# Performance work log

Hardware: AMD Instinct MI355X
Metric: run time of the kernel (lower is better)

The kernel has to match this reference:

```python
import jax, jax.numpy as jnp
import numpy as np

H = 128  # hidden size
I = 256  # input size

def setup_inputs() -> dict:
    key = jax.random.key(0)
    ks = jax.random.split(key, 12)
    s_ih = 1.0 / np.sqrt(H)
    inp = {
        "x": jax.random.normal(ks[0], (256, 512, I), dtype=jnp.float32),
        # PyTorch LSTM params, gate order (i, f, g, o)
        "W_ih": jax.random.uniform(ks[1], (4 * H, I), jnp.float32, -s_ih, s_ih),
        "W_hh": jax.random.uniform(ks[2], (4 * H, H), jnp.float32, -s_ih, s_ih),
        "b_ih": jax.random.uniform(ks[3], (4 * H,), jnp.float32, -s_ih, s_ih),
        "b_hh": jax.random.uniform(ks[4], (4 * H,), jnp.float32, -s_ih, s_ih),
        "W1": jax.random.uniform(ks[5], (64, H), jnp.float32, -1/np.sqrt(H), 1/np.sqrt(H)),
        "b1": jax.random.uniform(ks[6], (64,), jnp.float32, -1/np.sqrt(H), 1/np.sqrt(H)),
        "W2": jax.random.uniform(ks[7], (32, 64), jnp.float32, -1/np.sqrt(64), 1/np.sqrt(64)),
        "b2": jax.random.uniform(ks[8], (32,), jnp.float32, -1/np.sqrt(64), 1/np.sqrt(64)),
        "W3": jax.random.uniform(ks[9], (4, 32), jnp.float32, -1/np.sqrt(32), 1/np.sqrt(32)),
        "b3": jax.random.uniform(ks[10], (4,), jnp.float32, -1/np.sqrt(32), 1/np.sqrt(32)),
    }
    return inp

def _lstm_last_hidden(x, W_ih, W_hh, b_ih, b_hh):
    B = x.shape[0]
    # Precompute input contribution for all timesteps: [B, T, 4H]
    gx = jnp.einsum("bti,gi->btg", x, W_ih) + (b_ih + b_hh)
    gx = jnp.swapaxes(gx, 0, 1)  # [T, B, 4H] for scan over time

    def step(carry, g_x):
        h, c = carry
        gates = g_x + h @ W_hh.T  # [B, 4H]
        i, f, g, o = jnp.split(gates, 4, axis=-1)
        i = jax.nn.sigmoid(i)
        f = jax.nn.sigmoid(f)
        g = jnp.tanh(g)
        o = jax.nn.sigmoid(o)
        c = f * c + i * g
        h = o * jnp.tanh(c)
        return (h, c), None

    h0 = jnp.zeros((B, H), x.dtype)
    (h, _), _ = jax.lax.scan(step, (h0, h0), gx)
    return h  # last-timestep hidden state [B, H]

def reference(x, W_ih, W_hh, b_ih, b_hh, W1, b1, W2, b2, W3, b3):
    h = _lstm_last_hidden(x, W_ih, W_hh, b_ih, b_hh)
    h = jax.nn.relu(h @ W1.T + b1)
    h = jax.nn.relu(h @ W2.T + b2)
    return h @ W3.T + b3  # [B, 4]
```

## Files before the change

kernel.cpp:

```cpp
#include <hip/hip_runtime.h>
#include <hip/hip_bf16.h>


#define TC       64
#define NCHUNK   8
#define BATCH    256
#define TSEQ     512
#define ISZ      256
#define HSZ      128
#define RB       4
#define NBLK     (BATCH / RB)
#define NGB      (2 * TC * 4)
#define HROW     144
#define GX_PER_T 131072
#define GXCH     ((size_t)TC * GX_PER_T)
#define STRT     32768
#define PF       4

#define XN       (BATCH * TSEQ * ISZ)
#define WIHN     (4 * HSZ * ISZ)
#define WHHN     (4 * HSZ * HSZ)
#define NCB      ((XN + WIHN + WHHN) / 8192)

typedef __attribute__((ext_vector_type(8))) short short8;
typedef __attribute__((ext_vector_type(4))) float f32x4;

__device__ __forceinline__ void barrier_nodrain() {
    __asm__ __volatile__("s_waitcnt lgkmcnt(0)\n\ts_barrier" ::: "memory");
}

__device__ __forceinline__ float fast_rcp(float x) {
    return __builtin_amdgcn_rcpf(x);
}
__device__ __forceinline__ float sigmoidf_(float x) {
    return fast_rcp(1.0f + __expf(-x));
}
__device__ __forceinline__ float tanhf_(float x) {
    float e = __expf(2.0f * x);
    return 1.0f - 2.0f * fast_rcp(e + 1.0f);
}
__device__ __forceinline__ unsigned short f2bf(float x) {
    union { float f; unsigned u; } v; v.f = x;
    unsigned r = v.u + 0x7fffu + ((v.u >> 16) & 1u);
    return (unsigned short)(r >> 16);
}
__device__ __forceinline__ float bf2f(unsigned short b) {
    union { unsigned u; float f; } v;
    v.u = ((unsigned)b) << 16;
    return v.f;
}
__device__ __forceinline__ unsigned packbf(float lo, float hi) {
    __hip_bfloat162 h2 = __float22bfloat162_rn(make_float2(lo, hi));
    union { __hip_bfloat162 h; unsigned u; } v; v.h = h2;
    return v.u;
}
__device__ __forceinline__ float sel4(f32x4 v, int r) {
    float s01 = (r & 1) ? v[1] : v[0];
    float s23 = (r & 1) ? v[3] : v[2];
    return (r & 2) ? s23 : s01;
}

__global__ __launch_bounds__(512, 2) void fused_kernel(
    const float* __restrict__ x, const float* __restrict__ Wih,
    const float* __restrict__ bih, const float* __restrict__ bhh,
    const float* __restrict__ Whh,
    const unsigned short* __restrict__ gxl, unsigned short* __restrict__ gxg,
    float* __restrict__ hc,
    unsigned short* __restrict__ xb, unsigned short* __restrict__ wihb,
    unsigned short* __restrict__ whhb,
    int t0, int first, int run_lstm, int run_gemm, int use_xbf, int run_conv)
{
    __shared__ __align__(16) char smem[32768];
    const int tid  = threadIdx.x;
    const int w    = tid >> 6;
    const int lane = tid & 63;
    const int n    = lane & 15;
    const int quad = lane >> 4;

    if (blockIdx.x >= NBLK + NGB) {
        if (!run_conv) return;
        const int cb = (int)blockIdx.x - (NBLK + NGB);
        const size_t e0 = ((size_t)cb * 512 + tid) * 16;
        const float* s; unsigned short* d;
        if (e0 < (size_t)XN)              { s = x + e0;                d = xb + e0; }
        else if (e0 < (size_t)(XN + WIHN)){ s = Wih + (e0 - XN);       d = wihb + (e0 - XN); }
        else                              { s = Whh + (e0 - XN - WIHN); d = whhb + (e0 - XN - WIHN); }
        float4 f0 = *(const float4*)(s);
        float4 f1 = *(const float4*)(s + 4);
        float4 f2 = *(const float4*)(s + 8);
        float4 f3 = *(const float4*)(s + 12);
        *(uint4*)(d)     = (uint4){packbf(f0.x, f0.y), packbf(f0.z, f0.w),
                                   packbf(f1.x, f1.y), packbf(f1.z, f1.w)};
        *(uint4*)(d + 8) = (uint4){packbf(f2.x, f2.y), packbf(f2.z, f2.w),
                                   packbf(f3.x, f3.y), packbf(f3.z, f3.w)};
        return;
    }

    if (blockIdx.x >= NBLK) {
        if (!run_gemm) return;
        short* As = (short*)smem;
        short* Bs = (short*)(smem + 16384);

        const int gb = (int)blockIdx.x - NBLK;
        const int nt = gb & 3;
        const int mt = gb >> 2;
        const int tl = mt >> 1;
        const int b0 = (mt & 1) * 128;
        const int n0 = nt * 128;

        const int mq = w & 1;
        const int nq = w >> 1;

        const int srow = tid >> 2;
        const int skh  = (tid & 3) * 8;

        f32x4 acc[4][2];
#pragma unroll
        for (int mi = 0; mi < 4; ++mi)
#pragma unroll
            for (int ni = 0; ni < 2; ++ni)
                acc[mi][ni] = (f32x4){0.f, 0.f, 0.f, 0.f};

        if (use_xbf) {
            const unsigned short* xr = xb + ((size_t)(b0 + srow) * TSEQ + (size_t)(t0 + tl)) * ISZ + skh;
            const unsigned short* wr = wihb + (size_t)(n0 + srow) * ISZ + skh;
            *(short8*)(&As[srow * 32 + skh]) = *(const short8*)(xr);
            *(short8*)(&Bs[srow * 32 + skh]) = *(const short8*)(wr);
            barrier_nodrain();
            for (int ks = 0; ks < 8; ++ks) {
                const int cur = (ks & 1) * 4096;
                const int nxt = 4096 - cur;
                short8 va, vb;
                if (ks < 7) {
                    va = *(const short8*)(xr + (ks + 1) * 32);
                    vb = *(const short8*)(wr + (ks + 1) * 32);
                }
                short8 af[4], bfr[2];
#pragma unroll
                for (int mi = 0; mi < 4; ++mi)
                    af[mi] = *(const short8*)(&As[cur + (mq * 64 + mi * 16 + n) * 32 + quad * 8]);
#pragma unroll
                for (int ni = 0; ni < 2; ++ni)
                    bfr[ni] = *(const short8*)(&Bs[cur + (nq * 32 + ni * 16 + n) * 32 + quad * 8]);
#pragma unroll
                for (int mi = 0; mi < 4; ++mi)
#pragma unroll
                    for (int ni = 0; ni < 2; ++ni)
                        acc[mi][ni] = __builtin_amdgcn_mfma_f32_16x16x32_bf16(
                            af[mi], bfr[ni], acc[mi][ni], 0, 0, 0);
                if (ks < 7) {
                    *(short8*)(&As[nxt + srow * 32 + skh]) = va;
                    *(short8*)(&Bs[nxt + srow * 32 + skh]) = vb;
                }
                barrier_nodrain();
            }
        } else {
            const float* xrow = x + ((size_t)(b0 + srow) * TSEQ + (size_t)(t0 + tl)) * ISZ + skh;
            const float* wrow = Wih + (size_t)(n0 + srow) * ISZ + skh;
            {
                float4 pa0 = *(const float4*)(xrow);
                float4 pa1 = *(const float4*)(xrow + 4);
                float4 pb0 = *(const float4*)(wrow);
                float4 pb1 = *(const float4*)(wrow + 4);
                *(uint4*)(&As[srow * 32 + skh]) =
                    (uint4){packbf(pa0.x, pa0.y), packbf(pa0.z, pa0.w),
                            packbf(pa1.x, pa1.y), packbf(pa1.z, pa1.w)};
                *(uint4*)(&Bs[srow * 32 + skh]) =
                    (uint4){packbf(pb0.x, pb0.y), packbf(pb0.z, pb0.w),
                            packbf(pb1.x, pb1.y), packbf(pb1.z, pb1.w)};
            }
            barrier_nodrain();
            for (int ks = 0; ks < 8; ++ks) {
                const int cur = (ks & 1) * 4096;
                const int nxt = 4096 - cur;
                float4 pa0, pa1, pb0, pb1;
                if (ks < 7) {
                    pa0 = *(const float4*)(xrow + (ks + 1) * 32);
                    pa1 = *(const float4*)(xrow + (ks + 1) * 32 + 4);
                    pb0 = *(const float4*)(wrow + (ks + 1) * 32);
                    pb1 = *(const float4*)(wrow + (ks + 1) * 32 + 4);
                }
                short8 af[4], bfr[2];
#pragma unroll
                for (int mi = 0; mi < 4; ++mi)
                    af[mi] = *(const short8*)(&As[cur + (mq * 64 + mi * 16 + n) * 32 + quad * 8]);
#pragma unroll
                for (int ni = 0; ni < 2; ++ni)
                    bfr[ni] = *(const short8*)(&Bs[cur + (nq * 32 + ni * 16 + n) * 32 + quad * 8]);
#pragma unroll
                for (int mi = 0; mi < 4; ++mi)
#pragma unroll
                    for (int ni = 0; ni < 2; ++ni)
                        acc[mi][ni] = __builtin_amdgcn_mfma_f32_16x16x32_bf16(
                            af[mi], bfr[ni], acc[mi][ni], 0, 0, 0);
                if (ks < 7) {
                    *(uint4*)(&As[nxt + srow * 32 + skh]) =
                        (uint4){packbf(pa0.x, pa0.y), packbf(pa0.z, pa0.w),
                                packbf(pa1.x, pa1.y), packbf(pa1.z, pa1.w)};
                    *(uint4*)(&Bs[nxt + srow * 32 + skh]) =
                        (uint4){packbf(pb0.x, pb0.y), packbf(pb0.z, pb0.w),
                                packbf(pb1.x, pb1.y), packbf(pb1.z, pb1.w)};
                }
                barrier_nodrain();
            }
        }

#pragma unroll
        for (int ni = 0; ni < 2; ++ni) {
            const int j    = nq * 32 + ni * 16 + n;
            const int gate = n0 + j;
            const float bias = bih[gate] + bhh[gate];
            const int wj = nq * 2 + ni;
#pragma unroll
            for (int mi = 0; mi < 4; ++mi) {
                const int bb   = b0 + mq * 64 + mi * 16 + quad * 4;
                const int blk2 = bb >> 2;
                const size_t idx = ((((size_t)nt * TC + tl) * 64 + blk2) * 512) +
                                   (size_t)wj * 64 + (size_t)n * 4;
                const unsigned lo = packbf(acc[mi][ni][0] + bias, acc[mi][ni][1] + bias);
                const unsigned hi = packbf(acc[mi][ni][2] + bias, acc[mi][ni][3] + bias);
                *(uint2*)(&gxg[idx]) = (uint2){lo, hi};
            }
        }
        return;
    }

    if (!run_lstm) return;
    __builtin_amdgcn_s_setprio(1);
    short* h_lds = (short*)smem;

    const int blk  = (int)blockIdx.x;
    const int b0   = blk * RB;
    const int nb   = lane & 3;
    const int jl   = lane >> 2;
    const int j    = 16 * w + jl;
    const int rsel = jl & 3;

    short8 Af[4][4];
#pragma unroll
    for (int g = 0; g < 4; ++g) {
        const unsigned short* rowb = whhb + (size_t)(128 * g + 16 * w + n) * HSZ + 8 * quad;
#pragma unroll
        for (int ks = 0; ks < 4; ++ks)
            Af[g][ks] = *(const short8*)(rowb + 32 * ks);
    }

    float c1 = 0.f, hl1 = 0.f;
    {
        unsigned short h0 = 0;
        if (!first) {
            c1 = hc[(size_t)BATCH * HSZ + (size_t)(b0 + nb) * HSZ + j];
            h0 = f2bf(hc[(size_t)(b0 + nb) * HSZ + j]);
        }
        *(unsigned short*)&h_lds[nb * HROW + j] = h0;
    }

    const unsigned short* gp[4];
#pragma unroll
    for (int g = 0; g < 4; ++g)
        gp[g] = gxl + (((size_t)g * TC) * 64 + blk) * 512 + (size_t)w * 64 + lane;

    unsigned short gq[PF][4];
#pragma unroll
    for (int d = 0; d < PF; ++d)
#pragma unroll
        for (int g = 0; g < 4; ++g)
            gq[d][g] = gp[g][(size_t)d * STRT];

    barrier_nodrain();

    for (int t = 0; t < TC; t += PF) {
#pragma unroll
        for (int u = 0; u < PF; ++u) {
            const int tt = t + u;
            const short* hb_r = h_lds + (u & 1) * (RB * HROW);
            short*       hb_w = h_lds + ((u & 1) ^ 1) * (RB * HROW);

            short8 Bf[4];
#pragma unroll
            for (int ks = 0; ks < 4; ++ks)
                Bf[ks] = *(const short8*)(&hb_r[nb * HROW + 32 * ks + 8 * quad]);

            f32x4 acc[4];
#pragma unroll
            for (int g = 0; g < 4; ++g)
                acc[g] = __builtin_amdgcn_mfma_f32_16x16x32_bf16(
                    Af[g][0], Bf[0], (f32x4){0.f, 0.f, 0.f, 0.f}, 0, 0, 0);
#pragma unroll
            for (int ks = 1; ks < 4; ++ks)
#pragma unroll
                for (int g = 0; g < 4; ++g)
                    acc[g] = __builtin_amdgcn_mfma_f32_16x16x32_bf16(
                        Af[g][ks], Bf[ks], acc[g], 0, 0, 0);

            const float s0 = sel4(acc[0], rsel) + bf2f(gq[u][0]);
            const float s1 = sel4(acc[1], rsel) + bf2f(gq[u][1]);
            const float s2 = sel4(acc[2], rsel) + bf2f(gq[u][2]);
            const float s3 = sel4(acc[3], rsel) + bf2f(gq[u][3]);

            const int tf = (tt + PF < TC) ? (tt + PF) : (TC - 1);
#pragma unroll
            for (int g = 0; g < 4; ++g)
                gq[u][g] = gp[g][(size_t)tf * STRT];

            const float ig = sigmoidf_(s0);
            const float fg = sigmoidf_(s1);
            const float gg = tanhf_(s2);
            const float og = sigmoidf_(s3);
            c1  = fg * c1 + ig * gg;
            hl1 = og * tanhf_(c1);

            *(unsigned short*)&hb_w[nb * HROW + j] = f2bf(hl1);
            barrier_nodrain();
        }
    }

    hc[(size_t)(b0 + nb) * HSZ + j] = hl1;
    hc[(size_t)BATCH * HSZ + (size_t)(b0 + nb) * HSZ + j] = c1;
}

__global__ __launch_bounds__(64) void head_kernel(
    const float* __restrict__ hc,
    const float* __restrict__ W1, const float* __restrict__ b1,
    const float* __restrict__ W2, const float* __restrict__ b2,
    const float* __restrict__ W3, const float* __restrict__ b3,
    float* __restrict__ out)
{
    __shared__ float hs[HSZ];
    __shared__ float o1[64];
    __shared__ float o2[32];
    const int bidx = blockIdx.x;
    const int t = threadIdx.x;
    hs[t]      = hc[bidx * HSZ + t];
    hs[t + 64] = hc[bidx * HSZ + t + 64];
    __syncthreads();
    {
        float a = b1[t];
#pragma unroll 8
        for (int k = 0; k < HSZ; ++k) a += W1[t * HSZ + k] * hs[k];
        o1[t] = fmaxf(a, 0.0f);
    }
    __syncthreads();
    if (t < 32) {
        float a = b2[t];
#pragma unroll 8
        for (int k = 0; k < 64; ++k) a += W2[t * 64 + k] * o1[k];
        o2[t] = fmaxf(a, 0.0f);
    }
    __syncthreads();
    if (t < 4) {
        float a = b3[t];
#pragma unroll
        for (int k = 0; k < 32; ++k) a += W3[t * 32 + k] * o2[k];
        out[bidx * 4 + t] = a;
    }
}

extern "C" void kernel_launch(void* const* d_in, const int* in_sizes, int n_in,
                              void* d_out, int out_size, void* d_ws, size_t ws_size,
                              hipStream_t stream) {
    const float* x   = (const float*)d_in[0];
    const float* Wih = (const float*)d_in[1];
    const float* Whh = (const float*)d_in[2];
    const float* bih = (const float*)d_in[3];
    const float* bhh = (const float*)d_in[4];
    const float* W1  = (const float*)d_in[5];
    const float* b1  = (const float*)d_in[6];
    const float* W2  = (const float*)d_in[7];
    const float* b2  = (const float*)d_in[8];
    const float* W3  = (const float*)d_in[9];
    const float* b3  = (const float*)d_in[10];
    float* out = (float*)d_out;

    const size_t GXB = GXCH * sizeof(unsigned short);
    unsigned short* gx0 = (unsigned short*)d_ws;
    unsigned short* gx1 = (unsigned short*)((char*)d_ws + GXB);
    float* hc = (float*)((char*)d_ws + 2 * GXB);
    unsigned short* xb   = (unsigned short*)((char*)d_ws + 2 * GXB + 262144);
    unsigned short* wihb = xb + (size_t)XN;
    unsigned short* whhb = wihb + WIHN;

    fused_kernel<<<dim3(NBLK + NGB + NCB), 512, 0, stream>>>(
        x, Wih, bih, bhh, Whh, gx0, gx0, hc, xb, wihb, whhb,
        0, 1, 0, 1, 0, 1);

    for (int c = 0; c < NCHUNK; ++c) {
        unsigned short* gl = (c & 1) ? gx1 : gx0;
        unsigned short* gg = (c & 1) ? gx0 : gx1;
        fused_kernel<<<dim3(NBLK + NGB), 512, 0, stream>>>(
            x, Wih, bih, bhh, Whh, gl, gg, hc, xb, wihb, whhb,
            (c + 1) * TC, c == 0 ? 1 : 0, 1, (c + 1) < NCHUNK ? 1 : 0, 1, 0);
    }

    head_kernel<<<dim3(BATCH), 64, 0, stream>>>(hc, W1, b1, W2, b2, W3, b3, out);
}
```

Before: 555.4 us.

## Split LSTM batch rows into two ping-pong groups to overlap MFMA with gates

The recurrent LSTM step now splits the 4 batch rows per block into two groups of 2. The MFMA for one group is issued while the gate nonlinearities of the other group run, so the two halves form a software pipeline across barriers. The gate-input prefetch now uses packed uint2 loads with two slots instead of scalar bf16 loads with a depth-4 queue. The prologue interleaves GEMM and conversion blocks in one grid, and the occupancy hint is raised to 4 blocks. Risks are extra barriers per step, redundant lanes that compute but do not write, and register pressure from the higher occupancy bound.

```diff
diff --git a/kernel.cpp b/kernel.cpp
--- a/kernel.cpp
+++ b/kernel.cpp
@@ -15,12 +15,12 @@
 #define GX_PER_T 131072
 #define GXCH     ((size_t)TC * GX_PER_T)
 #define STRT     32768
-#define PF       4
 
 #define XN       (BATCH * TSEQ * ISZ)
 #define WIHN     (4 * HSZ * ISZ)
 #define WHHN     (4 * HSZ * HSZ)
 #define NCB      ((XN + WIHN + WHHN) / 8192)
+#define GRID_PRO 4632
 
 typedef __attribute__((ext_vector_type(8))) short short8;
 typedef __attribute__((ext_vector_type(4))) float f32x4;
@@ -44,9 +44,9 @@
     unsigned r = v.u + 0x7fffu + ((v.u >> 16) & 1u);
     return (unsigned short)(r >> 16);
 }
-__device__ __forceinline__ float bf2f(unsigned short b) {
+__device__ __forceinline__ float bfhalf(unsigned wv, int hi) {
     union { unsigned u; float f; } v;
-    v.u = ((unsigned)b) << 16;
+    v.u = hi ? (wv & 0xffff0000u) : (wv << 16);
     return v.f;
 }
 __device__ __forceinline__ unsigned packbf(float lo, float hi) {
@@ -60,7 +60,7 @@
     return (r & 2) ? s23 : s01;
 }
 
-__global__ __launch_bounds__(512, 2) void fused_kernel(
+__global__ __launch_bounds__(512, 4) void fused_kernel(
     const float* __restrict__ x, const float* __restrict__ Wih,
     const float* __restrict__ bih, const float* __restrict__ bhh,
     const float* __restrict__ Whh,
@@ -68,7 +68,7 @@
     float* __restrict__ hc,
     unsigned short* __restrict__ xb, unsigned short* __restrict__ wihb,
     unsigned short* __restrict__ whhb,
-    int t0, int first, int run_lstm, int run_gemm, int use_xbf, int run_conv)
+    int t0, int first, int run_lstm, int run_gemm, int use_xbf, int prologue)
 {
     __shared__ __align__(16) char smem[32768];
     const int tid  = threadIdx.x;
@@ -77,13 +77,27 @@
     const int n    = lane & 15;
     const int quad = lane >> 4;
 
-    if (blockIdx.x >= NBLK + NGB) {
-        if (!run_conv) return;
-        const int cb = (int)blockIdx.x - (NBLK + NGB);
-        const size_t e0 = ((size_t)cb * 512 + tid) * 16;
+    int gemm_gb = -1, conv_cb = -1, lstm_blk = -1;
+    {
+        const int idx = (int)blockIdx.x;
+        if (prologue) {
+            if (idx < 4096) {
+                if ((idx & 7) == 0) gemm_gb = idx >> 3;
+                else                conv_cb = idx - (idx >> 3) - 1;
+            } else if (idx < GRID_PRO) {
+                conv_cb = 3584 + (idx - 4096);
+            } else return;
+        } else {
+            if (idx < NBLK) lstm_blk = idx;
+            else            gemm_gb  = idx - NBLK;
+        }
+    }
+
+    if (conv_cb >= 0) {
+        const size_t e0 = ((size_t)conv_cb * 512 + tid) * 16;
         const float* s; unsigned short* d;
-        if (e0 < (size_t)XN)              { s = x + e0;                d = xb + e0; }
-        else if (e0 < (size_t)(XN + WIHN)){ s = Wih + (e0 - XN);       d = wihb + (e0 - XN); }
+        if (e0 < (size_t)XN)              { s = x + e0;                 d = xb + e0; }
+        else if (e0 < (size_t)(XN + WIHN)){ s = Wih + (e0 - XN);        d = wihb + (e0 - XN); }
         else                              { s = Whh + (e0 - XN - WIHN); d = whhb + (e0 - XN - WIHN); }
         float4 f0 = *(const float4*)(s);
         float4 f1 = *(const float4*)(s + 4);
@@ -96,12 +110,12 @@
         return;
     }
 
-    if (blockIdx.x >= NBLK) {
+    if (gemm_gb >= 0) {
         if (!run_gemm) return;
         short* As = (short*)smem;
         short* Bs = (short*)(smem + 16384);
 
-        const int gb = (int)blockIdx.x - NBLK;
+        const int gb = gemm_gb;
         const int nt = gb & 3;
         const int mt = gb >> 2;
         const int tl = mt >> 1;
@@ -229,12 +243,13 @@
     __builtin_amdgcn_s_setprio(1);
     short* h_lds = (short*)smem;
 
-    const int blk  = (int)blockIdx.x;
-    const int b0   = blk * RB;
-    const int nb   = lane & 3;
-    const int jl   = lane >> 2;
-    const int j    = 16 * w + jl;
-    const int rsel = jl & 3;
+    const int blk   = lstm_blk;
+    const int b0    = blk * RB;
+    const int jl    = lane >> 2;
+    const int j     = 16 * w + jl;
+    const int rsel  = jl & 3;
+    const int bsel  = lane & 1;
+    const bool wlane = (lane & 2) == 0;
 
     short8 Af[4][4];
 #pragma unroll
@@ -245,78 +260,109 @@
             Af[g][ks] = *(const short8*)(rowb + 32 * ks);
     }
 
-    float c1 = 0.f, hl1 = 0.f;
-    {
-        unsigned short h0 = 0;
+    float cst[2], hl[2];
+#pragma unroll
+    for (int g = 0; g < 2; ++g) {
+        const int b = 2 * g + bsel;
+        float cv = 0.f; unsigned short h0 = 0;
         if (!first) {
-            c1 = hc[(size_t)BATCH * HSZ + (size_t)(b0 + nb) * HSZ + j];
-            h0 = f2bf(hc[(size_t)(b0 + nb) * HSZ + j]);
+            cv = hc[(size_t)BATCH * HSZ + (size_t)(b0 + b) * HSZ + j];
+            h0 = f2bf(hc[(size_t)(b0 + b) * HSZ + j]);
         }
-        *(unsigned short*)&h_lds[nb * HROW + j] = h0;
-    }
-
-    const unsigned short* gp[4];
-#pragma unroll
-    for (int g = 0; g < 4; ++g)
-        gp[g] = gxl + (((size_t)g * TC) * 64 + blk) * 512 + (size_t)w * 64 + lane;
-
-    unsigned short gq[PF][4];
-#pragma unroll
-    for (int d = 0; d < PF; ++d)
-#pragma unroll
-        for (int g = 0; g < 4; ++g)
-            gq[d][g] = gp[g][(size_t)d * STRT];
+        cst[g] = cv; hl[g] = 0.f;
+        if (wlane) *(unsigned short*)&h_lds[b * HROW + j] = h0;
+    }
+
+    const unsigned short* gbase = gxl + (size_t)blk * 512 + w * 64 + 4 * jl;
+    uint2 gq[2][4];
+#pragma unroll
+    for (int s = 0; s < 2; ++s)
+#pragma unroll
+        for (int p = 0; p < 4; ++p)
+            gq[s][p] = *(const uint2*)(gbase + ((size_t)p * TC + s) * STRT);
 
     barrier_nodrain();
 
-    for (int t = 0; t < TC; t += PF) {
-#pragma unroll
-        for (int u = 0; u < PF; ++u) {
-            const int tt = t + u;
-            const short* hb_r = h_lds + (u & 1) * (RB * HROW);
-            short*       hb_w = h_lds + ((u & 1) ^ 1) * (RB * HROW);
-
-            short8 Bf[4];
-#pragma unroll
-            for (int ks = 0; ks < 4; ++ks)
-                Bf[ks] = *(const short8*)(&hb_r[nb * HROW + 32 * ks + 8 * quad]);
-
-            f32x4 acc[4];
-#pragma unroll
-            for (int g = 0; g < 4; ++g)
-                acc[g] = __builtin_amdgcn_mfma_f32_16x16x32_bf16(
-                    Af[g][0], Bf[0], (f32x4){0.f, 0.f, 0.f, 0.f}, 0, 0, 0);
-#pragma unroll
-            for (int ks = 1; ks < 4; ++ks)
-#pragma unroll
-                for (int g = 0; g < 4; ++g)
-                    acc[g] = __builtin_amdgcn_mfma_f32_16x16x32_bf16(
-                        Af[g][ks], Bf[ks], acc[g], 0, 0, 0);
-
-            const float s0 = sel4(acc[0], rsel) + bf2f(gq[u][0]);
-            const float s1 = sel4(acc[1], rsel) + bf2f(gq[u][1]);
-            const float s2 = sel4(acc[2], rsel) + bf2f(gq[u][2]);
-            const float s3 = sel4(acc[3], rsel) + bf2f(gq[u][3]);
-
-            const int tf = (tt + PF < TC) ? (tt + PF) : (TC - 1);
-#pragma unroll
-            for (int g = 0; g < 4; ++g)
-                gq[u][g] = gp[g][(size_t)tf * STRT];
-
-            const float ig = sigmoidf_(s0);
-            const float fg = sigmoidf_(s1);
-            const float gg = tanhf_(s2);
-            const float og = sigmoidf_(s3);
-            c1  = fg * c1 + ig * gg;
-            hl1 = og * tanhf_(c1);
-
-            *(unsigned short*)&hb_w[nb * HROW + j] = f2bf(hl1);
-            barrier_nodrain();
+    f32x4 aP0[4], aP1[4];
+
+#define MF_PHASE(grp, A)                                                      \
+    do {                                                                      \
+        const short* hb_ = h_lds + (2 * (grp) + bsel) * HROW;                 \
+        _Pragma("unroll")                                                     \
+        for (int ks_ = 0; ks_ < 4; ++ks_) {                                   \
+            short8 Bf_ = *(const short8*)(hb_ + 32 * ks_ + 8 * quad);         \
+            if (ks_ == 0) {                                                   \
+                _Pragma("unroll")                                             \
+                for (int g_ = 0; g_ < 4; ++g_)                                \
+                    A[g_] = __builtin_amdgcn_mfma_f32_16x16x32_bf16(          \
+                        Af[g_][0], Bf_, (f32x4){0.f, 0.f, 0.f, 0.f}, 0, 0, 0);\
+            } else {                                                          \
+                _Pragma("unroll")                                             \
+                for (int g_ = 0; g_ < 4; ++g_)                                \
+                    A[g_] = __builtin_amdgcn_mfma_f32_16x16x32_bf16(          \
+                        Af[g_][ks_], Bf_, A[g_], 0, 0, 0);                    \
+            }                                                                 \
+        }                                                                     \
+    } while (0)
+
+#define GATES_PHASE(grp, A, S)                                                \
+    do {                                                                      \
+        const float s0_ = sel4(A[0], rsel) + bfhalf((grp) ? (S)[0].y : (S)[0].x, bsel); \
+        const float s1_ = sel4(A[1], rsel) + bfhalf((grp) ? (S)[1].y : (S)[1].x, bsel); \
+        const float s2_ = sel4(A[2], rsel) + bfhalf((grp) ? (S)[2].y : (S)[2].x, bsel); \
+        const float s3_ = sel4(A[3], rsel) + bfhalf((grp) ? (S)[3].y : (S)[3].x, bsel); \
+        const float ig_ = sigmoidf_(s0_);                                     \
+        const float fg_ = sigmoidf_(s1_);                                     \
+        const float gg_ = tanhf_(s2_);                                        \
+        const float og_ = sigmoidf_(s3_);                                     \
+        cst[grp] = fg_ * cst[grp] + ig_ * gg_;                                \
+        hl[grp]  = og_ * tanhf_(cst[grp]);                                    \
+        if (wlane)                                                            \
+            *(unsigned short*)&h_lds[(2 * (grp) + bsel) * HROW + j] = f2bf(hl[grp]); \
+    } while (0)
+
+#define RELOAD_SLOT(S, tf_)                                                   \
+    do {                                                                      \
+        const int tc_ = ((tf_) < TC) ? (tf_) : (TC - 1);                      \
+        _Pragma("unroll")                                                     \
+        for (int p_ = 0; p_ < 4; ++p_)                                        \
+            gq[S][p_] = *(const uint2*)(gbase + ((size_t)p_ * TC + tc_) * STRT); \
+    } while (0)
+
+    MF_PHASE(0, aP0);
+    barrier_nodrain();
+
+    for (int t = 0; t < TC; t += 2) {
+        MF_PHASE(1, aP1);
+        GATES_PHASE(0, aP0, gq[0]);
+        barrier_nodrain();
+
+        MF_PHASE(0, aP0);
+        GATES_PHASE(1, aP1, gq[0]);
+        RELOAD_SLOT(0, t + 2);
+        barrier_nodrain();
+
+        MF_PHASE(1, aP1);
+        GATES_PHASE(0, aP0, gq[1]);
+        barrier_nodrain();
+
+        MF_PHASE(0, aP0);
+        GATES_PHASE(1, aP1, gq[1]);
+        RELOAD_SLOT(1, t + 3);
+        barrier_nodrain();
+    }
+
+#pragma unroll
+    for (int g = 0; g < 2; ++g) {
+        const int b = 2 * g + bsel;
+        if (wlane) {
+            hc[(size_t)(b0 + b) * HSZ + j] = hl[g];
+            hc[(size_t)BATCH * HSZ + (size_t)(b0 + b) * HSZ + j] = cst[g];
         }
     }
-
-    hc[(size_t)(b0 + nb) * HSZ + j] = hl1;
-    hc[(size_t)BATCH * HSZ + (size_t)(b0 + nb) * HSZ + j] = c1;
+#undef MF_PHASE
+#undef GATES_PHASE
+#undef RELOAD_SLOT
 }
 
 __global__ __launch_bounds__(64) void head_kernel(
@@ -380,7 +426,7 @@
     unsigned short* wihb = xb + (size_t)XN;
     unsigned short* whhb = wihb + WIHN;
 
-    fused_kernel<<<dim3(NBLK + NGB + NCB), 512, 0, stream>>>(
+    fused_kernel<<<dim3(GRID_PRO), 512, 0, stream>>>(
         x, Wih, bih, bhh, Whh, gx0, gx0, hc, xb, wihb, whhb,
         0, 1, 0, 1, 0, 1);
 
```

After: 1.215 ms. 2.19x slower.
